# Kernel optimization log

Measured on AMD Instinct MI355X. Metric: run time of the kernel, lower is better.

Reference implementation:

```python
import jax, jax.numpy as jnp
import numpy as np

NUM_WIRES = 20
BATCH = 32
DIM = 2 ** NUM_WIRES


def setup_inputs() -> dict:
    key = jax.random.key(0)
    k1, k2, k3 = jax.random.split(key, 3)
    state = jax.random.normal(k1, (BATCH, DIM), dtype=jnp.float32)
    state = state / jnp.linalg.norm(state, axis=1, keepdims=True)  # valid quantum states
    params = jax.random.normal(k2, (2 * NUM_WIRES,), dtype=jnp.float32)
    W = jax.random.normal(k3, (1, NUM_WIRES), dtype=jnp.float32) * 0.1
    b = jnp.zeros((1,), dtype=jnp.float32)
    return {"state": state, "params": params, "W": W, "b": b}


def _apply_1q(psi, U, wire):
    # psi: [B, 2^n] complex; apply 2x2 unitary U on `wire` (wire 0 = most significant axis,
    # matching PennyLane's big-endian wire ordering).
    B = psi.shape[0]
    left = 2 ** wire
    psi4 = psi.reshape(B, left, 2, -1)
    psi4 = jnp.einsum('ts,bisj->bitj', U, psi4)
    return psi4.reshape(B, DIM)


def _apply_cnot(psi, ctrl):
    # CNOT on adjacent wires (ctrl, ctrl+1): swap target amplitudes where control=1.
    B = psi.shape[0]
    left = 2 ** ctrl
    psi5 = psi.reshape(B, left, 2, 2, -1)
    top = psi5[:, :, 0]
    bot = psi5[:, :, 1, ::-1]
    return jnp.stack([top, bot], axis=2).reshape(B, DIM)


def _circuit(state, params):
    psi = state.astype(jnp.complex64)
    for i in range(NUM_WIRES):
        # RX(theta_i)
        c = jnp.cos(params[i] / 2).astype(jnp.complex64)
        s = jnp.sin(params[i] / 2)
        RX = jnp.stack([jnp.stack([c, -1j * s]), jnp.stack([-1j * s, c])])
        psi = _apply_1q(psi, RX, i)
        # RY(theta_{i+n})
        c2 = jnp.cos(params[i + NUM_WIRES] / 2).astype(jnp.complex64)
        s2 = jnp.sin(params[i + NUM_WIRES] / 2).astype(jnp.complex64)
        RY = jnp.stack([jnp.stack([c2, -s2]), jnp.stack([s2, c2])])
        psi = _apply_1q(psi, RY, i)
    for i in range(NUM_WIRES - 1):
        psi = _apply_cnot(psi, i)
    # <Z_i> = sum over basis states of |amp|^2 * (+1 if bit_i==0 else -1)
    probs = psi.real ** 2 + psi.imag ** 2  # [B, 2^n] float32
    B = probs.shape[0]
    feats = []
    for i in range(NUM_WIRES):
        p = probs.reshape(B, 2 ** i, 2, -1)
        feats.append(p[:, :, 0].sum(axis=(1, 2)) - p[:, :, 1].sum(axis=(1, 2)))
    return jnp.stack(feats, axis=1)  # [B, n]


def reference(state, params, W, b):
    feats = _circuit(state, params)          # [B, num_wires]
    out = feats @ W.T + b                    # Linear head
    return out.squeeze(-1)                   # [B]
```

## Files before the change

### kernel.cpp

```cpp
#include <hip/hip_runtime.h>
#include <hip/hip_fp16.h>

#define NW    20
#define BATCH 32

struct PkW { __half2 A, Dp, Dn, E, En, F; };

__device__ __forceinline__ __half2 h2swap(__half2 v) {
    __half2 r; r.x = v.y; r.y = v.x; return r;
}

__device__ __forceinline__ __half2 pkrtz(float lo, float hi) {
    typedef __fp16 f16x2 __attribute__((ext_vector_type(2)));
    f16x2 v = __builtin_amdgcn_cvt_pkrtz(lo, hi);
    return *reinterpret_cast<__half2*>(&v);
}

__device__ __forceinline__ void bflyh(__half2& x0, __half2& x1, const PkW& u) {
    __half2 s0 = h2swap(x0), s1 = h2swap(x1);
    __half2 n0 = __hfma2(u.A, x0, __hfma2(u.Dp, s0, __hfma2(u.En, x1, __hmul2(u.F,  s1))));
    __half2 n1 = __hfma2(u.E, x0, __hfma2(u.F,  s0, __hfma2(u.A,  x1, __hmul2(u.Dn, s1))));
    x0 = n0; x1 = n1;
}

template<int JB>
__device__ __forceinline__ void stage16h(__half2 (&x)[16], const PkW& u) {
    #pragma unroll
    for (int base = 0; base < 16; ++base)
        if (!(base & (1 << JB)))
            bflyh(x[base], x[base | (1 << JB)], u);
}

__global__ void setupk(const float* __restrict__ params, float* __restrict__ cbuf) {
    int w = threadIdx.x;
    if (w < NW) {
        double s1, c1, s2, c2;
        sincos(0.5 * (double)params[w],      &s1, &c1);
        sincos(0.5 * (double)params[w + NW], &s2, &c2);
        float a = (float)(c1 * c2), d = (float)(s1 * s2);
        float e = (float)(s2 * c1), f = (float)(c2 * s1);
        if (w == 19) {
            cbuf[0] = a * 1024.f; cbuf[1] = d * 1024.f;
            cbuf[2] = e * 1024.f; cbuf[3] = f * 1024.f;
        }
        PkW pw;
        pw.A  = __floats2half2_rn( a,  a);
        pw.Dp = __floats2half2_rn(-d,  d);
        pw.Dn = __floats2half2_rn( d, -d);
        pw.E  = __floats2half2_rn( e,  e);
        pw.En = __floats2half2_rn(-e, -e);
        pw.F  = __floats2half2_rn( f, -f);
        ((PkW*)(cbuf + 4))[w] = pw;
    }
}

__global__ __launch_bounds__(256, 8) void pass1(const float* __restrict__ state,
                                                const float* __restrict__ cbuf,
                                                __half2* __restrict__ amp) {
    __shared__ __half2 lh[4224];
    const int t     = threadIdx.x;
    const int b     = blockIdx.x >> 8;
    const int chunk = blockIdx.x & 255;
    const PkW* PW = (const PkW*)(cbuf + 4);
    const float a19 = cbuf[0], d19 = cbuf[1], e19 = cbuf[2], f19 = cbuf[3];

    const float4* src = (const float4*)(state + ((size_t)b << 20) + ((size_t)chunk << 12));
    float u[16];
    #pragma unroll
    for (int k = 0; k < 4; ++k) {
        float4 v = src[k * 256 + t];
        u[k*4+0] = v.x; u[k*4+1] = v.y; u[k*4+2] = v.z; u[k*4+3] = v.w;
    }
    __half2 x[16];
    #pragma unroll
    for (int r = 0; r < 16; r += 2) {
        float u0 = u[r], u1 = u[r + 1];
        x[r]     = pkrtz(fmaf(a19, u0, -e19 * u1), fmaf( d19, u0, -f19 * u1));
        x[r + 1] = pkrtz(fmaf(e19, u0,  a19 * u1), fmaf(-f19, u0, -d19 * u1));
    }
    {
        const PkW uw18 = PW[18], uw9 = PW[9], uw8 = PW[8];
        stage16h<1>(x, uw18);
        stage16h<2>(x, uw9);
        stage16h<3>(x, uw8);
    }
    {
        const int p1 = 4 * t + (t >> 3);
        #pragma unroll
        for (int r = 0; r < 16; ++r)
            lh[p1 + (r & 3) + 1056 * (r >> 2)] = x[r];
    }
    __syncthreads();

    const int p2 = (t & 3) + 66 * (t >> 2);
    #pragma unroll
    for (int r = 0; r < 16; ++r) {
        const int c = 4 * (r & 3) + 16 * (r >> 2);
        x[r] = lh[p2 + c + (c >> 5)];
    }
    {
        const PkW uw17 = PW[17], uw16 = PW[16], uw15 = PW[15], uw14 = PW[14];
        stage16h<0>(x, uw17);
        stage16h<1>(x, uw16);
        stage16h<2>(x, uw15);
        stage16h<3>(x, uw14);
    }
    #pragma unroll
    for (int r = 0; r < 16; ++r) {
        const int c = 4 * (r & 3) + 16 * (r >> 2);
        lh[p2 + c + (c >> 5)] = x[r];
    }
    __syncthreads();

    const int p3 = (t & 63) + ((t & 63) >> 5) + 1056 * (t >> 6);
    #pragma unroll
    for (int r = 0; r < 16; ++r)
        x[r] = lh[p3 + 66 * (r & 3) + 264 * (r >> 2)];
    {
        const PkW uw13 = PW[13], uw12 = PW[12], uw11 = PW[11], uw10 = PW[10];
        stage16h<0>(x, uw13);
        stage16h<1>(x, uw12);
        stage16h<2>(x, uw11);
        stage16h<3>(x, uw10);
    }

    __half2* dst = amp + ((size_t)b << 20) + ((size_t)chunk << 12);
    const int sbase = (t & 63) + 1024 * (t >> 6);
    #pragma unroll
    for (int r = 0; r < 16; ++r)
        dst[sbase + 64 * (r & 3) + 256 * (r >> 2)] = x[r];
}

__global__ __launch_bounds__(256, 8) void pass2(const __half2* __restrict__ amp,
                                                const float* __restrict__ cbuf,
                                                const float* __restrict__ Wv,
                                                float* __restrict__ pws) {
    __shared__ __half2 lh[4224];
    __shared__ float2  Asig[256];
    __shared__ float   Btab[16];
    __shared__ float   wred[4];
    const int t        = threadIdx.x;
    const int b        = blockIdx.x >> 8;
    const int chunk    = blockIdx.x & 255;
    const int low_base = chunk * 16;
    const int l = t & 15, hi = t >> 4;
    const PkW* PW = (const PkW*)(cbuf + 4);

    {
        float A = 0.f;
        #pragma unroll
        for (int i = 0; i < 8; ++i)
            A += Wv[i] * (1.f - 2.f * (float)(__popc(t >> (7 - i)) & 1));
        Asig[t] = make_float2(A, 1.f - 2.f * (float)(__popc(t) & 1));
    }
    if (t < 16) {
        int low = low_base + t;
        float Bs = 0.f;
        #pragma unroll
        for (int i = 8; i < 20; ++i)
            Bs += Wv[i] * (1.f - 2.f * (float)(__popc(low >> (19 - i)) & 1));
        Btab[t] = Bs;
    }

    const __half2* src = amp + ((size_t)b << 20) + low_base + l;
    __half2 x[16];
    #pragma unroll
    for (int r = 0; r < 16; ++r)
        x[r] = src[(size_t)(hi * 16 + r) * 4096];
    {
        const PkW uw7 = PW[7], uw6 = PW[6], uw5 = PW[5], uw4 = PW[4];
        stage16h<0>(x, uw7);
        stage16h<1>(x, uw6);
        stage16h<2>(x, uw5);
        stage16h<3>(x, uw4);
    }
    {
        const int p = 264 * hi + l;
        #pragma unroll
        for (int r = 0; r < 16; ++r)
            lh[p + 16 * r + (r >> 1)] = x[r];
    }
    __syncthreads();
    {
        const int p = t + (t >> 5);
        #pragma unroll
        for (int r = 0; r < 16; ++r)
            x[r] = lh[p + 264 * r];
    }
    {
        const PkW uw3 = PW[3], uw2 = PW[2], uw1 = PW[1], uw0 = PW[0];
        stage16h<0>(x, uw3);
        stage16h<1>(x, uw2);
        stage16h<2>(x, uw1);
        stage16h<3>(x, uw0);
    }

    const float Bl = Btab[l];
    float acc = 0.f;
    #pragma unroll
    for (int r = 0; r < 16; ++r) {
        float2 v  = __half22float2(x[r]);
        float2 as = Asig[r * 16 + hi];
        acc = fmaf(fmaf(v.x, v.x, v.y * v.y), fmaf(as.y, Bl, as.x), acc);
    }
    #pragma unroll
    for (int off = 32; off > 0; off >>= 1) acc += __shfl_down(acc, off, 64);
    if ((t & 63) == 0) wred[t >> 6] = acc;
    __syncthreads();
    if (t == 0) pws[blockIdx.x] = (wred[0] + wred[1]) + (wred[2] + wred[3]);
}

__global__ void finalk(const float* __restrict__ pws, const float* __restrict__ bias,
                       float* __restrict__ out) {
    const int t = threadIdx.x;
    const int b = t >> 3, j = t & 7;
    float s = 0.f;
    #pragma unroll 4
    for (int k = 0; k < 32; ++k) s += pws[b * 256 + j * 32 + k];
    s += __shfl_down(s, 4, 8);
    s += __shfl_down(s, 2, 8);
    s += __shfl_down(s, 1, 8);
    if (j == 0) out[b] = s * (1.f / 1048576.f) + bias[0];
}

extern "C" void kernel_launch(void* const* d_in, const int* in_sizes, int n_in,
                              void* d_out, int out_size, void* d_ws, size_t ws_size,
                              hipStream_t stream) {
    const float* state  = (const float*)d_in[0];
    const float* params = (const float*)d_in[1];
    const float* Wv     = (const float*)d_in[2];
    const float* bias   = (const float*)d_in[3];
    float* out = (float*)d_out;

    __half2* amp  = (__half2*)d_ws;
    float*   pws  = (float*)((char*)d_ws + (size_t)BATCH * (1u << 20) * 4);
    float*   cbuf = (float*)((char*)d_ws + (size_t)BATCH * (1u << 20) * 4 + 8192 * 4);

    setupk<<<1, 64, 0, stream>>>(params, cbuf);
    pass1 <<<BATCH * 256, 256, 0, stream>>>(state, cbuf, amp);
    pass2 <<<BATCH * 256, 256, 0, stream>>>(amp, cbuf, Wv, pws);
    finalk<<<1, 256, 0, stream>>>(pws, bias, out);
}
```

Baseline: 120.3 us.

## Pack two batch elements per half2 lane in split real/imag layout

Each half2 lane now holds the same amplitude from two batch elements (b and b+16), with real and imaginary parts kept in separate register and LDS arrays. Before, one half2 held the real and imaginary parts of one amplitude. The butterfly no longer needs the lane swaps and can use uniform packed coefficients, and each block handles two batch rows, so the grid is halved. The cost is twice the registers and LDS per thread, with launch bounds lowered to 4 waves to match. Partial sums are written per slot, and the final reduction is re-indexed to match.

After: 107.2 us. 10.8% less time.

```diff
diff --git a/kernel.cpp b/kernel.cpp
--- a/kernel.cpp
+++ b/kernel.cpp
@@ -4,31 +4,28 @@
 #define NW    20
 #define BATCH 32
 
-struct PkW { __half2 A, Dp, Dn, E, En, F; };
-
-__device__ __forceinline__ __half2 h2swap(__half2 v) {
-    __half2 r; r.x = v.y; r.y = v.x; return r;
-}
+struct PkW7 { __half2 a, d, dn, e, en, f, fn, pad; };
 
 __device__ __forceinline__ __half2 pkrtz(float lo, float hi) {
     typedef __fp16 f16x2 __attribute__((ext_vector_type(2)));
     f16x2 v = __builtin_amdgcn_cvt_pkrtz(lo, hi);
     return *reinterpret_cast<__half2*>(&v);
 }
-
-__device__ __forceinline__ void bflyh(__half2& x0, __half2& x1, const PkW& u) {
-    __half2 s0 = h2swap(x0), s1 = h2swap(x1);
-    __half2 n0 = __hfma2(u.A, x0, __hfma2(u.Dp, s0, __hfma2(u.En, x1, __hmul2(u.F,  s1))));
-    __half2 n1 = __hfma2(u.E, x0, __hfma2(u.F,  s0, __hfma2(u.A,  x1, __hmul2(u.Dn, s1))));
-    x0 = n0; x1 = n1;
-}
+__device__ __forceinline__ unsigned h2u(__half2 v) { return *reinterpret_cast<unsigned*>(&v); }
+__device__ __forceinline__ __half2 u2h(unsigned v) { return *reinterpret_cast<__half2*>(&v); }
 
 template<int JB>
-__device__ __forceinline__ void stage16h(__half2 (&x)[16], const PkW& u) {
+__device__ __forceinline__ void stage16s(__half2 (&xr)[16], __half2 (&xi)[16], const PkW7 u) {
     #pragma unroll
     for (int base = 0; base < 16; ++base)
-        if (!(base & (1 << JB)))
-            bflyh(x[base], x[base | (1 << JB)], u);
+        if (!(base & (1 << JB))) {
+            const int p = base | (1 << JB);
+            __half2 x0r = xr[base], x0i = xi[base], x1r = xr[p], x1i = xi[p];
+            xr[base] = __hfma2(u.a, x0r, __hfma2(u.dn, x0i, __hfma2(u.en, x1r, __hmul2(u.f , x1i))));
+            xi[base] = __hfma2(u.a, x0i, __hfma2(u.d , x0r, __hfma2(u.en, x1i, __hmul2(u.fn, x1r))));
+            xr[p]    = __hfma2(u.e, x0r, __hfma2(u.f , x0i, __hfma2(u.a , x1r, __hmul2(u.d , x1i))));
+            xi[p]    = __hfma2(u.e, x0i, __hfma2(u.fn, x0r, __hfma2(u.a , x1i, __hmul2(u.dn, x1r))));
+        }
 }
 
 __global__ void setupk(const float* __restrict__ params, float* __restrict__ cbuf) {
@@ -43,52 +40,61 @@
             cbuf[0] = a * 1024.f; cbuf[1] = d * 1024.f;
             cbuf[2] = e * 1024.f; cbuf[3] = f * 1024.f;
         }
-        PkW pw;
-        pw.A  = __floats2half2_rn( a,  a);
-        pw.Dp = __floats2half2_rn(-d,  d);
-        pw.Dn = __floats2half2_rn( d, -d);
-        pw.E  = __floats2half2_rn( e,  e);
-        pw.En = __floats2half2_rn(-e, -e);
-        pw.F  = __floats2half2_rn( f, -f);
-        ((PkW*)(cbuf + 4))[w] = pw;
-    }
-}
-
-__global__ __launch_bounds__(256, 8) void pass1(const float* __restrict__ state,
+        PkW7 pw;
+        pw.a  = __floats2half2_rn( a,  a);
+        pw.d  = __floats2half2_rn( d,  d);
+        pw.dn = __floats2half2_rn(-d, -d);
+        pw.e  = __floats2half2_rn( e,  e);
+        pw.en = __floats2half2_rn(-e, -e);
+        pw.f  = __floats2half2_rn( f,  f);
+        pw.fn = __floats2half2_rn(-f, -f);
+        pw.pad = __floats2half2_rn(0.f, 0.f);
+        ((PkW7*)(cbuf + 4))[w] = pw;
+    }
+}
+
+__global__ __launch_bounds__(256, 4) void pass1(const float* __restrict__ state,
                                                 const float* __restrict__ cbuf,
-                                                __half2* __restrict__ amp) {
-    __shared__ __half2 lh[4224];
+                                                uint2* __restrict__ amp) {
+    __shared__ __half2 Lr[4224];
+    __shared__ __half2 Li[4224];
     const int t     = threadIdx.x;
-    const int b     = blockIdx.x >> 8;
+    const int pr    = blockIdx.x >> 8;
     const int chunk = blockIdx.x & 255;
-    const PkW* PW = (const PkW*)(cbuf + 4);
+    const PkW7* PW = (const PkW7*)(cbuf + 4);
     const float a19 = cbuf[0], d19 = cbuf[1], e19 = cbuf[2], f19 = cbuf[3];
 
-    const float4* src = (const float4*)(state + ((size_t)b << 20) + ((size_t)chunk << 12));
-    float u[16];
+    const float4* s0 = (const float4*)(state + ((size_t)pr << 20) + ((size_t)chunk << 12));
+    const float4* s1 = (const float4*)((const float*)s0 + ((size_t)16 << 20));
+
+    __half2 xr[16], xi[16];
     #pragma unroll
     for (int k = 0; k < 4; ++k) {
-        float4 v = src[k * 256 + t];
-        u[k*4+0] = v.x; u[k*4+1] = v.y; u[k*4+2] = v.z; u[k*4+3] = v.w;
-    }
-    __half2 x[16];
-    #pragma unroll
-    for (int r = 0; r < 16; r += 2) {
-        float u0 = u[r], u1 = u[r + 1];
-        x[r]     = pkrtz(fmaf(a19, u0, -e19 * u1), fmaf( d19, u0, -f19 * u1));
-        x[r + 1] = pkrtz(fmaf(e19, u0,  a19 * u1), fmaf(-f19, u0, -d19 * u1));
-    }
-    {
-        const PkW uw18 = PW[18], uw9 = PW[9], uw8 = PW[8];
-        stage16h<1>(x, uw18);
-        stage16h<2>(x, uw9);
-        stage16h<3>(x, uw8);
-    }
+        float4 v0 = s0[k * 256 + t];
+        float4 v1 = s1[k * 256 + t];
+        float r0a = fmaf(a19, v0.x, -e19 * v0.y), i0a = fmaf( d19, v0.x, -f19 * v0.y);
+        float r1a = fmaf(e19, v0.x,  a19 * v0.y), i1a = fmaf(-f19, v0.x, -d19 * v0.y);
+        float r0b = fmaf(a19, v1.x, -e19 * v1.y), i0b = fmaf( d19, v1.x, -f19 * v1.y);
+        float r1b = fmaf(e19, v1.x,  a19 * v1.y), i1b = fmaf(-f19, v1.x, -d19 * v1.y);
+        xr[4*k+0] = pkrtz(r0a, r0b); xi[4*k+0] = pkrtz(i0a, i0b);
+        xr[4*k+1] = pkrtz(r1a, r1b); xi[4*k+1] = pkrtz(i1a, i1b);
+        r0a = fmaf(a19, v0.z, -e19 * v0.w); i0a = fmaf( d19, v0.z, -f19 * v0.w);
+        r1a = fmaf(e19, v0.z,  a19 * v0.w); i1a = fmaf(-f19, v0.z, -d19 * v0.w);
+        r0b = fmaf(a19, v1.z, -e19 * v1.w); i0b = fmaf( d19, v1.z, -f19 * v1.w);
+        r1b = fmaf(e19, v1.z,  a19 * v1.w); i1b = fmaf(-f19, v1.z, -d19 * v1.w);
+        xr[4*k+2] = pkrtz(r0a, r0b); xi[4*k+2] = pkrtz(i0a, i0b);
+        xr[4*k+3] = pkrtz(r1a, r1b); xi[4*k+3] = pkrtz(i1a, i1b);
+    }
+    stage16s<1>(xr, xi, PW[18]);
+    stage16s<2>(xr, xi, PW[9]);
+    stage16s<3>(xr, xi, PW[8]);
     {
         const int p1 = 4 * t + (t >> 3);
         #pragma unroll
-        for (int r = 0; r < 16; ++r)
-            lh[p1 + (r & 3) + 1056 * (r >> 2)] = x[r];
+        for (int r = 0; r < 16; ++r) {
+            const int a = p1 + (r & 3) + 1056 * (r >> 2);
+            Lr[a] = xr[r]; Li[a] = xi[r];
+        }
     }
     __syncthreads();
 
@@ -96,55 +102,56 @@
     #pragma unroll
     for (int r = 0; r < 16; ++r) {
         const int c = 4 * (r & 3) + 16 * (r >> 2);
-        x[r] = lh[p2 + c + (c >> 5)];
-    }
-    {
-        const PkW uw17 = PW[17], uw16 = PW[16], uw15 = PW[15], uw14 = PW[14];
-        stage16h<0>(x, uw17);
-        stage16h<1>(x, uw16);
-        stage16h<2>(x, uw15);
-        stage16h<3>(x, uw14);
-    }
+        const int a = p2 + c + (c >> 5);
+        xr[r] = Lr[a]; xi[r] = Li[a];
+    }
+    stage16s<0>(xr, xi, PW[17]);
+    stage16s<1>(xr, xi, PW[16]);
+    stage16s<2>(xr, xi, PW[15]);
+    stage16s<3>(xr, xi, PW[14]);
     #pragma unroll
     for (int r = 0; r < 16; ++r) {
         const int c = 4 * (r & 3) + 16 * (r >> 2);
-        lh[p2 + c + (c >> 5)] = x[r];
+        const int a = p2 + c + (c >> 5);
+        Lr[a] = xr[r]; Li[a] = xi[r];
     }
     __syncthreads();
 
     const int p3 = (t & 63) + ((t & 63) >> 5) + 1056 * (t >> 6);
     #pragma unroll
-    for (int r = 0; r < 16; ++r)
-        x[r] = lh[p3 + 66 * (r & 3) + 264 * (r >> 2)];
-    {
-        const PkW uw13 = PW[13], uw12 = PW[12], uw11 = PW[11], uw10 = PW[10];
-        stage16h<0>(x, uw13);
-        stage16h<1>(x, uw12);
-        stage16h<2>(x, uw11);
-        stage16h<3>(x, uw10);
-    }
-
-    __half2* dst = amp + ((size_t)b << 20) + ((size_t)chunk << 12);
+    for (int r = 0; r < 16; ++r) {
+        const int a = p3 + 66 * (r & 3) + 264 * (r >> 2);
+        xr[r] = Lr[a]; xi[r] = Li[a];
+    }
+    stage16s<0>(xr, xi, PW[13]);
+    stage16s<1>(xr, xi, PW[12]);
+    stage16s<2>(xr, xi, PW[11]);
+    stage16s<3>(xr, xi, PW[10]);
+
+    uint2* dst = amp + ((size_t)pr << 20) + ((size_t)chunk << 12);
     const int sbase = (t & 63) + 1024 * (t >> 6);
     #pragma unroll
-    for (int r = 0; r < 16; ++r)
-        dst[sbase + 64 * (r & 3) + 256 * (r >> 2)] = x[r];
-}
-
-__global__ __launch_bounds__(256, 8) void pass2(const __half2* __restrict__ amp,
+    for (int r = 0; r < 16; ++r) {
+        uint2 w; w.x = h2u(xr[r]); w.y = h2u(xi[r]);
+        dst[sbase + 64 * (r & 3) + 256 * (r >> 2)] = w;
+    }
+}
+
+__global__ __launch_bounds__(256, 4) void pass2(const uint2* __restrict__ amp,
                                                 const float* __restrict__ cbuf,
                                                 const float* __restrict__ Wv,
                                                 float* __restrict__ pws) {
-    __shared__ __half2 lh[4224];
+    __shared__ __half2 Lr[4224];
+    __shared__ __half2 Li[4224];
     __shared__ float2  Asig[256];
     __shared__ float   Btab[16];
-    __shared__ float   wred[4];
+    __shared__ float   wred[8];
     const int t        = threadIdx.x;
-    const int b        = blockIdx.x >> 8;
+    const int pr       = blockIdx.x >> 8;
     const int chunk    = blockIdx.x & 255;
     const int low_base = chunk * 16;
     const int l = t & 15, hi = t >> 4;
-    const PkW* PW = (const PkW*)(cbuf + 4);
+    const PkW7* PW = (const PkW7*)(cbuf + 4);
 
     {
         float A = 0.f;
@@ -162,61 +169,72 @@
         Btab[t] = Bs;
     }
 
-    const __half2* src = amp + ((size_t)b << 20) + low_base + l;
-    __half2 x[16];
-    #pragma unroll
-    for (int r = 0; r < 16; ++r)
-        x[r] = src[(size_t)(hi * 16 + r) * 4096];
-    {
-        const PkW uw7 = PW[7], uw6 = PW[6], uw5 = PW[5], uw4 = PW[4];
-        stage16h<0>(x, uw7);
-        stage16h<1>(x, uw6);
-        stage16h<2>(x, uw5);
-        stage16h<3>(x, uw4);
-    }
+    const uint2* src = amp + ((size_t)pr << 20) + low_base + l;
+    __half2 xr[16], xi[16];
+    #pragma unroll
+    for (int r = 0; r < 16; ++r) {
+        uint2 w = src[(size_t)(hi * 16 + r) * 4096];
+        xr[r] = u2h(w.x); xi[r] = u2h(w.y);
+    }
+    stage16s<0>(xr, xi, PW[7]);
+    stage16s<1>(xr, xi, PW[6]);
+    stage16s<2>(xr, xi, PW[5]);
+    stage16s<3>(xr, xi, PW[4]);
     {
         const int p = 264 * hi + l;
         #pragma unroll
-        for (int r = 0; r < 16; ++r)
-            lh[p + 16 * r + (r >> 1)] = x[r];
+        for (int r = 0; r < 16; ++r) {
+            const int a = p + 16 * r + (r >> 1);
+            Lr[a] = xr[r]; Li[a] = xi[r];
+        }
     }
     __syncthreads();
     {
         const int p = t + (t >> 5);
         #pragma unroll
-        for (int r = 0; r < 16; ++r)
-            x[r] = lh[p + 264 * r];
-    }
-    {
-        const PkW uw3 = PW[3], uw2 = PW[2], uw1 = PW[1], uw0 = PW[0];
-        stage16h<0>(x, uw3);
-        stage16h<1>(x, uw2);
-        stage16h<2>(x, uw1);
-        stage16h<3>(x, uw0);
-    }
+        for (int r = 0; r < 16; ++r) {
+            const int a = p + 264 * r;
+            xr[r] = Lr[a]; xi[r] = Li[a];
+        }
+    }
+    stage16s<0>(xr, xi, PW[3]);
+    stage16s<1>(xr, xi, PW[2]);
+    stage16s<2>(xr, xi, PW[1]);
+    stage16s<3>(xr, xi, PW[0]);
 
     const float Bl = Btab[l];
-    float acc = 0.f;
-    #pragma unroll
-    for (int r = 0; r < 16; ++r) {
-        float2 v  = __half22float2(x[r]);
+    float acc0 = 0.f, acc1 = 0.f;
+    #pragma unroll
+    for (int r = 0; r < 16; ++r) {
+        float2 vr = __half22float2(xr[r]);
+        float2 vi = __half22float2(xi[r]);
         float2 as = Asig[r * 16 + hi];
-        acc = fmaf(fmaf(v.x, v.x, v.y * v.y), fmaf(as.y, Bl, as.x), acc);
-    }
-    #pragma unroll
-    for (int off = 32; off > 0; off >>= 1) acc += __shfl_down(acc, off, 64);
-    if ((t & 63) == 0) wred[t >> 6] = acc;
-    __syncthreads();
-    if (t == 0) pws[blockIdx.x] = (wred[0] + wred[1]) + (wred[2] + wred[3]);
+        float g = fmaf(as.y, Bl, as.x);
+        acc0 = fmaf(fmaf(vr.x, vr.x, vi.x * vi.x), g, acc0);
+        acc1 = fmaf(fmaf(vr.y, vr.y, vi.y * vi.y), g, acc1);
+    }
+    #pragma unroll
+    for (int off = 32; off > 0; off >>= 1) {
+        acc0 += __shfl_down(acc0, off, 64);
+        acc1 += __shfl_down(acc1, off, 64);
+    }
+    if ((t & 63) == 0) { wred[(t >> 6) * 2] = acc0; wred[(t >> 6) * 2 + 1] = acc1; }
+    __syncthreads();
+    if (t < 2)
+        pws[blockIdx.x * 2 + t] = (wred[t] + wred[2 + t]) + (wred[4 + t] + wred[6 + t]);
 }
 
 __global__ void finalk(const float* __restrict__ pws, const float* __restrict__ bias,
                        float* __restrict__ out) {
     const int t = threadIdx.x;
     const int b = t >> 3, j = t & 7;
+    const int pr = b & 15, sl = b >> 4;
     float s = 0.f;
     #pragma unroll 4
-    for (int k = 0; k < 32; ++k) s += pws[b * 256 + j * 32 + k];
+    for (int k = 0; k < 32; ++k) {
+        const int c = j * 32 + k;
+        s += pws[(pr * 256 + c) * 2 + sl];
+    }
     s += __shfl_down(s, 4, 8);
     s += __shfl_down(s, 2, 8);
     s += __shfl_down(s, 1, 8);
@@ -232,12 +250,12 @@
     const float* bias   = (const float*)d_in[3];
     float* out = (float*)d_out;
 
-    __half2* amp  = (__half2*)d_ws;
-    float*   pws  = (float*)((char*)d_ws + (size_t)BATCH * (1u << 20) * 4);
-    float*   cbuf = (float*)((char*)d_ws + (size_t)BATCH * (1u << 20) * 4 + 8192 * 4);
+    uint2* amp  = (uint2*)d_ws;
+    float* pws  = (float*)((char*)d_ws + (size_t)16 * (1u << 20) * 8);
+    float* cbuf = (float*)((char*)d_ws + (size_t)16 * (1u << 20) * 8 + 8192 * 4);
 
     setupk<<<1, 64, 0, stream>>>(params, cbuf);
-    pass1 <<<BATCH * 256, 256, 0, stream>>>(state, cbuf, amp);
-    pass2 <<<BATCH * 256, 256, 0, stream>>>(amp, cbuf, Wv, pws);
+    pass1 <<<16 * 256, 256, 0, stream>>>(state, cbuf, amp);
+    pass2 <<<16 * 256, 256, 0, stream>>>(amp, cbuf, Wv, pws);
     finalk<<<1, 256, 0, stream>>>(pws, bias, out);
 }
```
